# Performance work log

Hardware: AMD Instinct MI355X
Metric: run time of the kernel (lower is better)

## Reference

```python
import jax, jax.numpy as jnp
import numpy as np

N = 50000
E = 800000
IN_C = 128
HID = 16
HEADS = 8
OUT_C = 64
NEG_SLOPE = 0.2


def setup_inputs() -> dict:
    key = jax.random.key(0)
    ks = jax.random.split(key, 12)
    x = jax.random.normal(ks[0], (N, IN_C), dtype=jnp.float32)
    edge_index = jax.random.randint(ks[1], (2, E), 0, N, dtype=jnp.int32)
    s = 0.1
    W1 = jax.random.normal(ks[2], (IN_C, HEADS * HID), dtype=jnp.float32) * s
    a1_src = jax.random.normal(ks[3], (HEADS, HID), dtype=jnp.float32) * s
    a1_dst = jax.random.normal(ks[4], (HEADS, HID), dtype=jnp.float32) * s
    b1 = jnp.zeros((HEADS * HID,), dtype=jnp.float32)
    W2 = jax.random.normal(ks[5], (HEADS * HID, OUT_C), dtype=jnp.float32) * s
    a2_src = jax.random.normal(ks[6], (1, OUT_C), dtype=jnp.float32) * s
    a2_dst = jax.random.normal(ks[7], (1, OUT_C), dtype=jnp.float32) * s
    b2 = jnp.zeros((OUT_C,), dtype=jnp.float32)
    return {"x": x, "edge_index": edge_index, "W1": W1, "a1_src": a1_src,
            "a1_dst": a1_dst, "b1": b1, "W2": W2, "a2_src": a2_src,
            "a2_dst": a2_dst, "b2": b2}


def gat_conv(x, src, dst, W, a_src, a_dst, b, heads, ch):
    # linear projection -> [N, H, C]
    h = (x @ W).reshape(N, heads, ch)
    # per-node attention logits [N, H]
    al_s = jnp.einsum('nhc,hc->nh', h, a_src)
    al_d = jnp.einsum('nhc,hc->nh', h, a_dst)
    # per-edge logits [E, H]
    e = jax.nn.leaky_relu(al_s[src] + al_d[dst], NEG_SLOPE)
    # segment softmax over incoming edges of each dst node
    emax = jax.ops.segment_max(e, dst, num_segments=N)
    ee = jnp.exp(e - emax[dst])
    denom = jax.ops.segment_sum(ee, dst, num_segments=N)
    alpha = ee / (denom[dst] + 1e-16)
    # weighted scatter-aggregate of source messages
    msg = h[src] * alpha[:, :, None]  # [E, H, C]
    out = jax.ops.segment_sum(msg, dst, num_segments=N)
    return out.reshape(N, heads * ch) + b


def reference(x, edge_index, W1, a1_src, a1_dst, b1, W2, a2_src, a2_dst, b2):
    # add self loops (PyG GATConv default add_self_loops=True)
    loops = jnp.arange(N, dtype=edge_index.dtype)
    src = jnp.concatenate([edge_index[0], loops])
    dst = jnp.concatenate([edge_index[1], loops])
    h = gat_conv(x, src, dst, W1, a1_src, a1_dst, b1, HEADS, HID)
    h = jax.nn.relu(h)
    # dropout p=0.6 is identity in eval mode
    out = gat_conv(h, src, dst, W2, a2_src, a2_dst, b2, 1, OUT_C)
    return out
```

## Files before the change

### kernel.cpp

```cpp
#include <hip/hip_runtime.h>
#include <hip/hip_fp16.h>
#include <math.h>

#define N_NODES 50000
#define E_EDGES 800000
#define IN_C    128
#define HID     16
#define HEADS   8
#define OUT_C   64
#define NEG_SLOPE 0.2f
#define CELLW   64

#define WCOLS   144
#define WSTRIDE 136
#define WBYTES  (WCOLS * WSTRIDE * 2)

typedef _Float16 half8 __attribute__((ext_vector_type(8)));
typedef _Float16 half4 __attribute__((ext_vector_type(4)));
typedef float floatx4 __attribute__((ext_vector_type(4)));

__device__ __forceinline__ float lrelu_exp(float v) {
    v = v > 0.f ? v : NEG_SLOPE * v;
    return __expf(v);
}

__device__ __forceinline__ void gload_lds16(const void* g, void* l) {
    __builtin_amdgcn_global_load_lds(
        (const __attribute__((address_space(1))) void*)g,
        (__attribute__((address_space(3))) void*)l, 16, 0, 0);
}

__global__ __launch_bounds__(256) void prep(
    const float* __restrict__ W1, const float* __restrict__ a1_src,
    const float* __restrict__ a1_dst, const float* __restrict__ W2,
    _Float16* __restrict__ W1t, _Float16* __restrict__ W2t,
    int* __restrict__ cursor) {
    const int t = threadIdx.x;
    const int n = blockIdx.x * 256 + t;
    if (n < N_NODES) cursor[n] = 0;
    if (blockIdx.x == 0) {
        const int col = t & 127;
        const int kq = (t >> 7) * 4;
        for (int it = 0; it < 16; ++it) {
            const int k0 = it * 8 + kq;
            half4 hv;
            hv[0] = (_Float16)W1[(size_t)(k0 + 0) * IN_C + col];
            hv[1] = (_Float16)W1[(size_t)(k0 + 1) * IN_C + col];
            hv[2] = (_Float16)W1[(size_t)(k0 + 2) * IN_C + col];
            hv[3] = (_Float16)W1[(size_t)(k0 + 3) * IN_C + col];
            *(half4*)&W1t[col * WSTRIDE + k0] = hv;
        }
    } else if (blockIdx.x == 1) {
        const int j = t & 15;
        const int k0 = (t >> 4) * 8;
        const float* av = (j < 8) ? (a1_src + j * 16) : (a1_dst + (j - 8) * 16);
        const int hc = (j & 7) * 16;
        for (int k = k0; k < k0 + 8; ++k) {
            float s = 0.f;
#pragma unroll
            for (int c = 0; c < 16; ++c) s += W1[(size_t)k * IN_C + hc + c] * av[c];
            W1t[(128 + j) * WSTRIDE + k] = (_Float16)s;
        }
    } else if (blockIdx.x == 2) {
        const int col = t & 63;
        const int kg = t >> 6;
        for (int k0 = kg * 32; k0 < kg * 32 + 32; k0 += 4) {
            half4 hv;
            hv[0] = (_Float16)W2[(size_t)(k0 + 0) * OUT_C + col];
            hv[1] = (_Float16)W2[(size_t)(k0 + 1) * OUT_C + col];
            hv[2] = (_Float16)W2[(size_t)(k0 + 2) * OUT_C + col];
            hv[3] = (_Float16)W2[(size_t)(k0 + 3) * OUT_C + col];
            *(half4*)&W2t[col * 136 + k0] = hv;
        }
    }
}

__global__ __launch_bounds__(256) void fused_gemm_fill(
    const float* __restrict__ X, const _Float16* __restrict__ W1t,
    __half* __restrict__ H,
    float* __restrict__ als, float* __restrict__ ald,
    const int* __restrict__ src, const int* __restrict__ dst,
    int* __restrict__ cursor, int* __restrict__ ell) {
    __shared__ _Float16 wT[WCOLS * WSTRIDE];
    const int bid = blockIdx.x;
    const int t = threadIdx.x;

    if (bid & 1) {
        const int tid = (bid >> 1) * 256 + t;
        if (tid < E_EDGES / 4) {
            const int4 s4 = ((const int4*)src)[tid];
            const int4 d4 = ((const int4*)dst)[tid];
            const int p0 = atomicAdd(&cursor[d4.x], 1);
            const int p1 = atomicAdd(&cursor[d4.y], 1);
            const int p2 = atomicAdd(&cursor[d4.z], 1);
            const int p3 = atomicAdd(&cursor[d4.w], 1);
            if (p0 < CELLW) ell[(size_t)d4.x * CELLW + p0] = s4.x;
            if (p1 < CELLW) ell[(size_t)d4.y * CELLW + p1] = s4.y;
            if (p2 < CELLW) ell[(size_t)d4.z * CELLW + p2] = s4.z;
            if (p3 < CELLW) ell[(size_t)d4.w * CELLW + p3] = s4.w;
        }
        return;
    }

    {
        const char* g = (const char*)W1t;
        char* l = (char*)wT;
        const int o = t * 16;
#pragma unroll
        for (int it = 0; it < 9; ++it) {
            const int off = it * 4096 + o;
            gload_lds16(g + off, l + off);
        }
        if (t < 144) {
            const int off = 36864 + o;
            gload_lds16(g + off, l + off);
        }
    }

    const int wave = t >> 6, lane = t & 63;
    const int m = lane & 15, quad = lane >> 4;
    const int r0w = (bid >> 1) * 64 + wave * 16;
    int rl = r0w + m;
    if (rl >= N_NODES) rl = N_NODES - 1;
    const float* Xr = X + (size_t)rl * IN_C;

    float4 xv[8];
#pragma unroll
    for (int kc = 0; kc < 4; ++kc) {
        const int k8 = kc * 32 + quad * 8;
        xv[kc * 2]     = *(const float4*)(Xr + k8);
        xv[kc * 2 + 1] = *(const float4*)(Xr + k8 + 4);
    }

    __syncthreads();

    floatx4 acc[9];
#pragma unroll
    for (int i = 0; i < 9; ++i) acc[i] = (floatx4){0.f, 0.f, 0.f, 0.f};

#pragma unroll
    for (int kc = 0; kc < 4; ++kc) {
        const int k8 = kc * 32 + quad * 8;
        const float4 xa = xv[kc * 2];
        const float4 xb = xv[kc * 2 + 1];
        half8 a;
        a[0] = (_Float16)xa.x; a[1] = (_Float16)xa.y;
        a[2] = (_Float16)xa.z; a[3] = (_Float16)xa.w;
        a[4] = (_Float16)xb.x; a[5] = (_Float16)xb.y;
        a[6] = (_Float16)xb.z; a[7] = (_Float16)xb.w;
#pragma unroll
        for (int ct = 0; ct < 9; ++ct) {
            const half8 b = *(const half8*)&wT[(ct * 16 + m) * WSTRIDE + k8];
            acc[ct] = __builtin_amdgcn_mfma_f32_16x16x32_f16(a, b, acc[ct], 0, 0, 0);
        }
    }

    _Float16* Hh = (_Float16*)H;
#pragma unroll
    for (int ct = 0; ct < 8; ++ct) {
#pragma unroll
        for (int r = 0; r < 4; ++r) {
            const int row = r0w + quad * 4 + r;
            if (row < N_NODES)
                Hh[(size_t)row * IN_C + ct * 16 + m] = (_Float16)acc[ct][r];
        }
    }
#pragma unroll
    for (int r = 0; r < 4; ++r) {
        const int row = r0w + quad * 4 + r;
        if (row < N_NODES) {
            if (m < 8) als[(size_t)row * HEADS + m] = acc[8][r];
            else       ald[(size_t)row * HEADS + (m - 8)] = acc[8][r];
        }
    }
}

__global__ __launch_bounds__(256) void agg1_gemm2(
    const int* __restrict__ cnt, const int* __restrict__ ell,
    const float* __restrict__ als, const float* __restrict__ ald,
    const __half* __restrict__ H, const float* __restrict__ b,
    const _Float16* __restrict__ W2t, const float* __restrict__ a2_src,
    const float* __restrict__ a2_dst, __half* __restrict__ H2,
    float* __restrict__ als2, float* __restrict__ ald2) {
    __shared__ _Float16 xrowh[16 * 136];
    __shared__ float l2buf[4][16][2];
    const int t = threadIdx.x;

    const int nl = t >> 4;
    const int h  = (t >> 1) & 7;
    const int e2 = t & 1;
    const int nc = blockIdx.x * 16 + nl;
    int deg = cnt[nc];
    deg = deg < CELLW ? deg : CELLW;
    const int* ep = ell + (size_t)nc * CELLW;
    const float ad = ald[nc * HEADS + h];
    float accv[16];
    float ssum;
    if (e2 == 0) {
        const float w = lrelu_exp(als[nc * HEADS + h] + ad);
        const half8* q = (const half8*)(H + ((size_t)nc * HEADS + h) * HID);
        const half8 u0 = q[0], u1 = q[1];
        ssum = w;
#pragma unroll
        for (int j = 0; j < 8; ++j) {
            accv[j] = w * (float)u0[j];
            accv[j + 8] = w * (float)u1[j];
        }
    } else {
        ssum = 0.f;
#pragma unroll
        for (int j = 0; j < 16; ++j) accv[j] = 0.f;
    }
    for (int p = 4 * e2; p < deg; p += 8) {
        const int4 s4 = *(const int4*)(ep + p);
        const int s0 = s4.x;
        const int i1 = (p + 1 < deg) ? s4.y : nc;
        const int i2 = (p + 2 < deg) ? s4.z : nc;
        const int i3 = (p + 3 < deg) ? s4.w : nc;
        const float f1 = (p + 1 < deg) ? 1.f : 0.f;
        const float f2 = (p + 2 < deg) ? 1.f : 0.f;
        const float f3 = (p + 3 < deg) ? 1.f : 0.f;
        const float v0 = als[s0 * HEADS + h];
        const float v1 = als[i1 * HEADS + h];
        const float v2 = als[i2 * HEADS + h];
        const float v3 = als[i3 * HEADS + h];
        const half8* q0 = (const half8*)(H + ((size_t)s0 * HEADS + h) * HID);
        const half8* q1 = (const half8*)(H + ((size_t)i1 * HEADS + h) * HID);
        const half8* q2 = (const half8*)(H + ((size_t)i2 * HEADS + h) * HID);
        const half8* q3 = (const half8*)(H + ((size_t)i3 * HEADS + h) * HID);
        const half8 a0 = q0[0], b0 = q0[1];
        const half8 a1 = q1[0], b1 = q1[1];
        const half8 a2 = q2[0], b2 = q2[1];
        const half8 a3 = q3[0], b3 = q3[1];
        const float w0 = lrelu_exp(v0 + ad);
        const float w1 = lrelu_exp(v1 + ad) * f1;
        const float w2 = lrelu_exp(v2 + ad) * f2;
        const float w3 = lrelu_exp(v3 + ad) * f3;
        ssum += (w0 + w1) + (w2 + w3);
#pragma unroll
        for (int j = 0; j < 8; ++j) {
            accv[j]     += w0 * (float)a0[j] + w1 * (float)a1[j] +
                           w2 * (float)a2[j] + w3 * (float)a3[j];
            accv[j + 8] += w0 * (float)b0[j] + w1 * (float)b1[j] +
                           w2 * (float)b2[j] + w3 * (float)b3[j];
        }
    }
    ssum += __shfl_xor(ssum, 1);
#pragma unroll
    for (int j = 0; j < 16; ++j) accv[j] += __shfl_xor(accv[j], 1);

    if (e2 == 0) {
        const float inv = 1.f / (ssum + 1e-16f);
        half8 r0, r1;
#pragma unroll
        for (int j = 0; j < 8; ++j) {
            float ra = accv[j] * inv + b[h * 16 + j];
            float rb = accv[j + 8] * inv + b[h * 16 + 8 + j];
            r0[j] = (_Float16)(ra > 0.f ? ra : 0.f);
            r1[j] = (_Float16)(rb > 0.f ? rb : 0.f);
        }
        _Float16* xr = &xrowh[nl * 136 + h * 16];
        *(half8*)(xr) = r0;
        *(half8*)(xr + 8) = r1;
    }

    __syncthreads();

    {
        const int wv = t >> 6, ln = t & 63;
        const int bm = ln & 15, quad = ln >> 4;
        floatx4 acc = (floatx4){0.f, 0.f, 0.f, 0.f};
        const _Float16* arow = &xrowh[bm * 136];
        const _Float16* brow = &W2t[(wv * 16 + bm) * 136];
#pragma unroll
        for (int kc = 0; kc < 4; ++kc) {
            const int k8 = kc * 32 + quad * 8;
            const half8 a  = *(const half8*)(arow + k8);
            const half8 bv = *(const half8*)(brow + k8);
            acc = __builtin_amdgcn_mfma_f32_16x16x32_f16(a, bv, acc, 0, 0, 0);
        }
        const float a2s = a2_src[wv * 16 + bm], a2d = a2_dst[wv * 16 + bm];
        _Float16* H2h = (_Float16*)H2;
        float psr[4], pdr[4];
#pragma unroll
        for (int r = 0; r < 4; ++r) {
            const float c = acc[r];
            float ps = c * a2s, pd = c * a2d;
            ps += __shfl_xor(ps, 1); pd += __shfl_xor(pd, 1);
            ps += __shfl_xor(ps, 2); pd += __shfl_xor(pd, 2);
            ps += __shfl_xor(ps, 4); pd += __shfl_xor(pd, 4);
            ps += __shfl_xor(ps, 8); pd += __shfl_xor(pd, 8);
            psr[r] = ps; pdr[r] = pd;
            const int row = blockIdx.x * 16 + quad * 4 + r;
            H2h[(size_t)row * OUT_C + wv * 16 + bm] = (_Float16)c;
        }
        if (bm == 0) {
#pragma unroll
            for (int r = 0; r < 4; ++r) {
                l2buf[wv][quad * 4 + r][0] = psr[r];
                l2buf[wv][quad * 4 + r][1] = pdr[r];
            }
        }
    }
    __syncthreads();
    if (t < 16) {
        const int n2 = blockIdx.x * 16 + t;
        als2[n2] = (l2buf[0][t][0] + l2buf[1][t][0]) + (l2buf[2][t][0] + l2buf[3][t][0]);
        ald2[n2] = (l2buf[0][t][1] + l2buf[1][t][1]) + (l2buf[2][t][1] + l2buf[3][t][1]);
    }
}

__global__ __launch_bounds__(256) void agg2(
    const int* __restrict__ cnt, const int* __restrict__ ell,
    const float* __restrict__ als, const float* __restrict__ ald,
    const __half* __restrict__ H, const float* __restrict__ b,
    float* __restrict__ out) {
    const int t = threadIdx.x;
    const int nl = t >> 4;
    const int jc = (t >> 1) & 7;
    const int e2 = t & 1;
    const int n = blockIdx.x * 16 + nl;
    const int j0 = jc * 8;
    int deg = cnt[n];
    deg = deg < CELLW ? deg : CELLW;
    const int* ep = ell + (size_t)n * CELLW;
    const float ad = ald[n];
    float accv[8];
    float ssum;
    if (e2 == 0) {
        const float w = lrelu_exp(als[n] + ad);
        const half8 u = *(const half8*)(H + (size_t)n * OUT_C + j0);
        ssum = w;
#pragma unroll
        for (int k = 0; k < 8; ++k) accv[k] = w * (float)u[k];
    } else {
        ssum = 0.f;
#pragma unroll
        for (int k = 0; k < 8; ++k) accv[k] = 0.f;
    }
    for (int p = 4 * e2; p < deg; p += 8) {
        const int4 s4 = *(const int4*)(ep + p);
        const int s0 = s4.x;
        const int i1 = (p + 1 < deg) ? s4.y : n;
        const int i2 = (p + 2 < deg) ? s4.z : n;
        const int i3 = (p + 3 < deg) ? s4.w : n;
        const float f1 = (p + 1 < deg) ? 1.f : 0.f;
        const float f2 = (p + 2 < deg) ? 1.f : 0.f;
        const float f3 = (p + 3 < deg) ? 1.f : 0.f;
        const float v0 = als[s0];
        const float v1 = als[i1];
        const float v2 = als[i2];
        const float v3 = als[i3];
        const half8 u0 = *(const half8*)(H + (size_t)s0 * OUT_C + j0);
        const half8 u1 = *(const half8*)(H + (size_t)i1 * OUT_C + j0);
        const half8 u2 = *(const half8*)(H + (size_t)i2 * OUT_C + j0);
        const half8 u3 = *(const half8*)(H + (size_t)i3 * OUT_C + j0);
        const float w0 = lrelu_exp(v0 + ad);
        const float w1 = lrelu_exp(v1 + ad) * f1;
        const float w2 = lrelu_exp(v2 + ad) * f2;
        const float w3 = lrelu_exp(v3 + ad) * f3;
        ssum += (w0 + w1) + (w2 + w3);
#pragma unroll
        for (int k = 0; k < 8; ++k)
            accv[k] += w0 * (float)u0[k] + w1 * (float)u1[k] +
                       w2 * (float)u2[k] + w3 * (float)u3[k];
    }
    ssum += __shfl_xor(ssum, 1);
#pragma unroll
    for (int k = 0; k < 8; ++k) accv[k] += __shfl_xor(accv[k], 1);

    if (e2 == 0) {
        const float inv = 1.f / (ssum + 1e-16f);
        floatx4 r0, r1;
        r0[0] = accv[0] * inv + b[j0 + 0]; r0[1] = accv[1] * inv + b[j0 + 1];
        r0[2] = accv[2] * inv + b[j0 + 2]; r0[3] = accv[3] * inv + b[j0 + 3];
        r1[0] = accv[4] * inv + b[j0 + 4]; r1[1] = accv[5] * inv + b[j0 + 5];
        r1[2] = accv[6] * inv + b[j0 + 6]; r1[3] = accv[7] * inv + b[j0 + 7];
        float* op = out + (size_t)n * OUT_C + j0;
        __builtin_nontemporal_store(r0, (floatx4*)op);
        __builtin_nontemporal_store(r1, (floatx4*)(op + 4));
    }
}

extern "C" void kernel_launch(void* const* d_in, const int* in_sizes, int n_in,
                              void* d_out, int out_size, void* d_ws, size_t ws_size,
                              hipStream_t stream) {
    const float* x      = (const float*)d_in[0];
    const int*   ei     = (const int*)d_in[1];
    const float* W1     = (const float*)d_in[2];
    const float* a1_src = (const float*)d_in[3];
    const float* a1_dst = (const float*)d_in[4];
    const float* b1     = (const float*)d_in[5];
    const float* W2     = (const float*)d_in[6];
    const float* a2_src = (const float*)d_in[7];
    const float* a2_dst = (const float*)d_in[8];
    const float* b2     = (const float*)d_in[9];
    const int* src = ei;
    const int* dst = ei + E_EDGES;
    float* outp = (float*)d_out;

    char* wsb = (char*)d_ws;
    __half* h1   = (__half*)wsb;
    __half* h2   = h1 + (size_t)N_NODES * IN_C;
    float*  als1 = (float*)(h2 + (size_t)N_NODES * OUT_C);
    float*  ald1 = als1 + N_NODES * HEADS;
    float*  als2 = ald1 + N_NODES * HEADS;
    float*  ald2 = als2 + N_NODES;
    int*    cursor = (int*)(ald2 + N_NODES);
    int*    ell    = cursor + N_NODES;
    _Float16* W2t  = (_Float16*)(ell + (size_t)N_NODES * CELLW);

    _Float16* W1t = (_Float16*)als2;

    prep<<<(N_NODES + 255) / 256, 256, 0, stream>>>(
        W1, a1_src, a1_dst, W2, W1t, W2t, cursor);

    {
        const int gemm_blocks = (N_NODES + 63) / 64;
        fused_gemm_fill<<<gemm_blocks * 2, 256, 0, stream>>>(
            x, W1t, h1, als1, ald1, src, dst, cursor, ell);
    }

    agg1_gemm2<<<N_NODES / 16, 256, 0, stream>>>(
        cursor, ell, als1, ald1, h1, b1, W2t, a2_src, a2_dst, h2, als2, ald2);

    agg2<<<N_NODES / 16, 256, 0, stream>>>(
        cursor, ell, als2, ald2, h2, b2, outp);
}
```

Before: 188.4 us.

## Pad ELL rows with a zero-weight phantom node and rebalance GEMM/fill blocks

Fills the whole ELL adjacency with a phantom node index and gives that node zero features and -1e30 attention logits. The aggregation loops can then drop per-edge bounds checks and masking multiplies, since padded slots contribute exp(-huge)=0. The fused GEMM/fill kernel now has each GEMM block handle 128 rows in two passes, with two edge-fill blocks per GEMM block. The price is a full 12.8 MB write of the ELL buffer in the prep kernel, plus padded workspace offsets.

```diff
diff --git a/kernel.cpp b/kernel.cpp
--- a/kernel.cpp
+++ b/kernel.cpp
@@ -10,10 +10,10 @@
 #define OUT_C   64
 #define NEG_SLOPE 0.2f
 #define CELLW   64
+#define PHANTOM N_NODES
 
 #define WCOLS   144
 #define WSTRIDE 136
-#define WBYTES  (WCOLS * WSTRIDE * 2)
 
 typedef _Float16 half8 __attribute__((ext_vector_type(8)));
 typedef _Float16 half4 __attribute__((ext_vector_type(4)));
@@ -34,10 +34,19 @@
     const float* __restrict__ W1, const float* __restrict__ a1_src,
     const float* __restrict__ a1_dst, const float* __restrict__ W2,
     _Float16* __restrict__ W1t, _Float16* __restrict__ W2t,
-    int* __restrict__ cursor) {
+    int* __restrict__ cursor, int* __restrict__ ell,
+    __half* __restrict__ H1, __half* __restrict__ H2,
+    float* __restrict__ als1, float* __restrict__ ald1,
+    float* __restrict__ als2) {
     const int t = threadIdx.x;
-    const int n = blockIdx.x * 256 + t;
-    if (n < N_NODES) cursor[n] = 0;
+    const int gid = blockIdx.x * 256 + t;
+    if (gid < N_NODES) cursor[gid] = 0;
+    {
+        const int4 pv = make_int4(PHANTOM, PHANTOM, PHANTOM, PHANTOM);
+        int4* e4 = (int4*)ell;
+        const int tot = N_NODES * CELLW / 4;
+        for (int i = gid; i < tot; i += gridDim.x * 256) e4[i] = pv;
+    }
     if (blockIdx.x == 0) {
         const int col = t & 127;
         const int kq = (t >> 7) * 4;
@@ -72,6 +81,13 @@
             hv[3] = (_Float16)W2[(size_t)(k0 + 3) * OUT_C + col];
             *(half4*)&W2t[col * 136 + k0] = hv;
         }
+    } else if (blockIdx.x == 3) {
+        const int4 z = make_int4(0, 0, 0, 0);
+        if (t < 16)      ((int4*)(H1 + (size_t)PHANTOM * IN_C))[t] = z;
+        else if (t < 24) ((int4*)(H2 + (size_t)PHANTOM * OUT_C))[t - 16] = z;
+        else if (t < 32) als1[(size_t)PHANTOM * HEADS + (t - 24)] = -1e30f;
+        else if (t < 40) ald1[(size_t)PHANTOM * HEADS + (t - 32)] = -1e30f;
+        else if (t == 40) als2[PHANTOM] = -1e30f;
     }
 }
 
@@ -84,9 +100,11 @@
     __shared__ _Float16 wT[WCOLS * WSTRIDE];
     const int bid = blockIdx.x;
     const int t = threadIdx.x;
-
-    if (bid & 1) {
-        const int tid = (bid >> 1) * 256 + t;
+    const int role = bid % 3;
+
+    if (role) {
+        const int fid = (bid / 3) * 2 + (role - 1);
+        const int tid = fid * 256 + t;
         if (tid < E_EDGES / 4) {
             const int4 s4 = ((const int4*)src)[tid];
             const int4 d4 = ((const int4*)dst)[tid];
@@ -117,60 +135,110 @@
         }
     }
 
+    const int g = bid / 3;
     const int wave = t >> 6, lane = t & 63;
     const int m = lane & 15, quad = lane >> 4;
-    const int r0w = (bid >> 1) * 64 + wave * 16;
-    int rl = r0w + m;
-    if (rl >= N_NODES) rl = N_NODES - 1;
-    const float* Xr = X + (size_t)rl * IN_C;
-
+    _Float16* Hh = (_Float16*)H;
+
+    const int r0a = g * 128 + wave * 16;
+    int rla = r0a + m;
+    if (rla >= N_NODES) rla = N_NODES - 1;
+    const float* Xra = X + (size_t)rla * IN_C;
     float4 xv[8];
 #pragma unroll
     for (int kc = 0; kc < 4; ++kc) {
         const int k8 = kc * 32 + quad * 8;
-        xv[kc * 2]     = *(const float4*)(Xr + k8);
-        xv[kc * 2 + 1] = *(const float4*)(Xr + k8 + 4);
+        xv[kc * 2]     = *(const float4*)(Xra + k8);
+        xv[kc * 2 + 1] = *(const float4*)(Xra + k8 + 4);
     }
 
     __syncthreads();
 
-    floatx4 acc[9];
-#pragma unroll
-    for (int i = 0; i < 9; ++i) acc[i] = (floatx4){0.f, 0.f, 0.f, 0.f};
-
-#pragma unroll
-    for (int kc = 0; kc < 4; ++kc) {
-        const int k8 = kc * 32 + quad * 8;
-        const float4 xa = xv[kc * 2];
-        const float4 xb = xv[kc * 2 + 1];
-        half8 a;
-        a[0] = (_Float16)xa.x; a[1] = (_Float16)xa.y;
-        a[2] = (_Float16)xa.z; a[3] = (_Float16)xa.w;
-        a[4] = (_Float16)xb.x; a[5] = (_Float16)xb.y;
-        a[6] = (_Float16)xb.z; a[7] = (_Float16)xb.w;
-#pragma unroll
-        for (int ct = 0; ct < 9; ++ct) {
-            const half8 b = *(const half8*)&wT[(ct * 16 + m) * WSTRIDE + k8];
-            acc[ct] = __builtin_amdgcn_mfma_f32_16x16x32_f16(a, b, acc[ct], 0, 0, 0);
-        }
-    }
-
-    _Float16* Hh = (_Float16*)H;
-#pragma unroll
-    for (int ct = 0; ct < 8; ++ct) {
+    {
+        floatx4 acc[9];
+#pragma unroll
+        for (int i = 0; i < 9; ++i) acc[i] = (floatx4){0.f, 0.f, 0.f, 0.f};
+#pragma unroll
+        for (int kc = 0; kc < 4; ++kc) {
+            const int k8 = kc * 32 + quad * 8;
+            const float4 xa = xv[kc * 2];
+            const float4 xb = xv[kc * 2 + 1];
+            half8 a;
+            a[0] = (_Float16)xa.x; a[1] = (_Float16)xa.y;
+            a[2] = (_Float16)xa.z; a[3] = (_Float16)xa.w;
+            a[4] = (_Float16)xb.x; a[5] = (_Float16)xb.y;
+            a[6] = (_Float16)xb.z; a[7] = (_Float16)xb.w;
+#pragma unroll
+            for (int ct = 0; ct < 9; ++ct) {
+                const half8 b = *(const half8*)&wT[(ct * 16 + m) * WSTRIDE + k8];
+                acc[ct] = __builtin_amdgcn_mfma_f32_16x16x32_f16(a, b, acc[ct], 0, 0, 0);
+            }
+        }
+#pragma unroll
+        for (int ct = 0; ct < 8; ++ct) {
+#pragma unroll
+            for (int r = 0; r < 4; ++r) {
+                const int row = r0a + quad * 4 + r;
+                if (row < N_NODES)
+                    Hh[(size_t)row * IN_C + ct * 16 + m] = (_Float16)acc[ct][r];
+            }
+        }
 #pragma unroll
         for (int r = 0; r < 4; ++r) {
-            const int row = r0w + quad * 4 + r;
-            if (row < N_NODES)
-                Hh[(size_t)row * IN_C + ct * 16 + m] = (_Float16)acc[ct][r];
-        }
-    }
-#pragma unroll
-    for (int r = 0; r < 4; ++r) {
-        const int row = r0w + quad * 4 + r;
-        if (row < N_NODES) {
-            if (m < 8) als[(size_t)row * HEADS + m] = acc[8][r];
-            else       ald[(size_t)row * HEADS + (m - 8)] = acc[8][r];
+            const int row = r0a + quad * 4 + r;
+            if (row < N_NODES) {
+                if (m < 8) als[(size_t)row * HEADS + m] = acc[8][r];
+                else       ald[(size_t)row * HEADS + (m - 8)] = acc[8][r];
+            }
+        }
+    }
+
+    {
+        const int r0b = r0a + 64;
+        int rlb = r0b + m;
+        if (rlb >= N_NODES) rlb = N_NODES - 1;
+        const float* Xrb = X + (size_t)rlb * IN_C;
+#pragma unroll
+        for (int kc = 0; kc < 4; ++kc) {
+            const int k8 = kc * 32 + quad * 8;
+            xv[kc * 2]     = *(const float4*)(Xrb + k8);
+            xv[kc * 2 + 1] = *(const float4*)(Xrb + k8 + 4);
+        }
+        floatx4 acc[9];
+#pragma unroll
+        for (int i = 0; i < 9; ++i) acc[i] = (floatx4){0.f, 0.f, 0.f, 0.f};
+#pragma unroll
+        for (int kc = 0; kc < 4; ++kc) {
+            const int k8 = kc * 32 + quad * 8;
+            const float4 xa = xv[kc * 2];
+            const float4 xb = xv[kc * 2 + 1];
+            half8 a;
+            a[0] = (_Float16)xa.x; a[1] = (_Float16)xa.y;
+            a[2] = (_Float16)xa.z; a[3] = (_Float16)xa.w;
+            a[4] = (_Float16)xb.x; a[5] = (_Float16)xb.y;
+            a[6] = (_Float16)xb.z; a[7] = (_Float16)xb.w;
+#pragma unroll
+            for (int ct = 0; ct < 9; ++ct) {
+                const half8 b = *(const half8*)&wT[(ct * 16 + m) * WSTRIDE + k8];
+                acc[ct] = __builtin_amdgcn_mfma_f32_16x16x32_f16(a, b, acc[ct], 0, 0, 0);
+            }
+        }
+#pragma unroll
+        for (int ct = 0; ct < 8; ++ct) {
+#pragma unroll
+            for (int r = 0; r < 4; ++r) {
+                const int row = r0b + quad * 4 + r;
+                if (row < N_NODES)
+                    Hh[(size_t)row * IN_C + ct * 16 + m] = (_Float16)acc[ct][r];
+            }
+        }
+#pragma unroll
+        for (int r = 0; r < 4; ++r) {
+            const int row = r0b + quad * 4 + r;
+            if (row < N_NODES) {
+                if (m < 8) als[(size_t)row * HEADS + m] = acc[8][r];
+                else       ald[(size_t)row * HEADS + (m - 8)] = acc[8][r];
+            }
         }
     }
 }
@@ -213,29 +281,22 @@
     }
     for (int p = 4 * e2; p < deg; p += 8) {
         const int4 s4 = *(const int4*)(ep + p);
-        const int s0 = s4.x;
-        const int i1 = (p + 1 < deg) ? s4.y : nc;
-        const int i2 = (p + 2 < deg) ? s4.z : nc;
-        const int i3 = (p + 3 < deg) ? s4.w : nc;
-        const float f1 = (p + 1 < deg) ? 1.f : 0.f;
-        const float f2 = (p + 2 < deg) ? 1.f : 0.f;
-        const float f3 = (p + 3 < deg) ? 1.f : 0.f;
-        const float v0 = als[s0 * HEADS + h];
-        const float v1 = als[i1 * HEADS + h];
-        const float v2 = als[i2 * HEADS + h];
-        const float v3 = als[i3 * HEADS + h];
-        const half8* q0 = (const half8*)(H + ((size_t)s0 * HEADS + h) * HID);
-        const half8* q1 = (const half8*)(H + ((size_t)i1 * HEADS + h) * HID);
-        const half8* q2 = (const half8*)(H + ((size_t)i2 * HEADS + h) * HID);
-        const half8* q3 = (const half8*)(H + ((size_t)i3 * HEADS + h) * HID);
+        const float v0 = als[s4.x * HEADS + h];
+        const float v1 = als[s4.y * HEADS + h];
+        const float v2 = als[s4.z * HEADS + h];
+        const float v3 = als[s4.w * HEADS + h];
+        const half8* q0 = (const half8*)(H + ((size_t)s4.x * HEADS + h) * HID);
+        const half8* q1 = (const half8*)(H + ((size_t)s4.y * HEADS + h) * HID);
+        const half8* q2 = (const half8*)(H + ((size_t)s4.z * HEADS + h) * HID);
+        const half8* q3 = (const half8*)(H + ((size_t)s4.w * HEADS + h) * HID);
         const half8 a0 = q0[0], b0 = q0[1];
         const half8 a1 = q1[0], b1 = q1[1];
         const half8 a2 = q2[0], b2 = q2[1];
         const half8 a3 = q3[0], b3 = q3[1];
         const float w0 = lrelu_exp(v0 + ad);
-        const float w1 = lrelu_exp(v1 + ad) * f1;
-        const float w2 = lrelu_exp(v2 + ad) * f2;
-        const float w3 = lrelu_exp(v3 + ad) * f3;
+        const float w1 = lrelu_exp(v1 + ad);
+        const float w2 = lrelu_exp(v2 + ad);
+        const float w3 = lrelu_exp(v3 + ad);
         ssum += (w0 + w1) + (w2 + w3);
 #pragma unroll
         for (int j = 0; j < 8; ++j) {
@@ -340,25 +401,18 @@
     }
     for (int p = 4 * e2; p < deg; p += 8) {
         const int4 s4 = *(const int4*)(ep + p);
-        const int s0 = s4.x;
-        const int i1 = (p + 1 < deg) ? s4.y : n;
-        const int i2 = (p + 2 < deg) ? s4.z : n;
-        const int i3 = (p + 3 < deg) ? s4.w : n;
-        const float f1 = (p + 1 < deg) ? 1.f : 0.f;
-        const float f2 = (p + 2 < deg) ? 1.f : 0.f;
-        const float f3 = (p + 3 < deg) ? 1.f : 0.f;
-        const float v0 = als[s0];
-        const float v1 = als[i1];
-        const float v2 = als[i2];
-        const float v3 = als[i3];
-        const half8 u0 = *(const half8*)(H + (size_t)s0 * OUT_C + j0);
-        const half8 u1 = *(const half8*)(H + (size_t)i1 * OUT_C + j0);
-        const half8 u2 = *(const half8*)(H + (size_t)i2 * OUT_C + j0);
-        const half8 u3 = *(const half8*)(H + (size_t)i3 * OUT_C + j0);
+        const float v0 = als[s4.x];
+        const float v1 = als[s4.y];
+        const float v2 = als[s4.z];
+        const float v3 = als[s4.w];
+        const half8 u0 = *(const half8*)(H + (size_t)s4.x * OUT_C + j0);
+        const half8 u1 = *(const half8*)(H + (size_t)s4.y * OUT_C + j0);
+        const half8 u2 = *(const half8*)(H + (size_t)s4.z * OUT_C + j0);
+        const half8 u3 = *(const half8*)(H + (size_t)s4.w * OUT_C + j0);
         const float w0 = lrelu_exp(v0 + ad);
-        const float w1 = lrelu_exp(v1 + ad) * f1;
-        const float w2 = lrelu_exp(v2 + ad) * f2;
-        const float w3 = lrelu_exp(v3 + ad) * f3;
+        const float w1 = lrelu_exp(v1 + ad);
+        const float w2 = lrelu_exp(v2 + ad);
+        const float w3 = lrelu_exp(v3 + ad);
         ssum += (w0 + w1) + (w2 + w3);
 #pragma unroll
         for (int k = 0; k < 8; ++k)
@@ -401,11 +455,11 @@
 
     char* wsb = (char*)d_ws;
     __half* h1   = (__half*)wsb;
-    __half* h2   = h1 + (size_t)N_NODES * IN_C;
-    float*  als1 = (float*)(h2 + (size_t)N_NODES * OUT_C);
-    float*  ald1 = als1 + N_NODES * HEADS;
-    float*  als2 = ald1 + N_NODES * HEADS;
-    float*  ald2 = als2 + N_NODES;
+    __half* h2   = h1 + (size_t)(N_NODES + 1) * IN_C;
+    float*  als1 = (float*)(h2 + (size_t)(N_NODES + 1) * OUT_C);
+    float*  ald1 = als1 + (size_t)(N_NODES + 1) * HEADS;
+    float*  als2 = ald1 + (size_t)(N_NODES + 1) * HEADS;
+    float*  ald2 = als2 + (N_NODES + 16);
     int*    cursor = (int*)(ald2 + N_NODES);
     int*    ell    = cursor + N_NODES;
     _Float16* W2t  = (_Float16*)(ell + (size_t)N_NODES * CELLW);
@@ -413,11 +467,11 @@
     _Float16* W1t = (_Float16*)als2;
 
     prep<<<(N_NODES + 255) / 256, 256, 0, stream>>>(
-        W1, a1_src, a1_dst, W2, W1t, W2t, cursor);
-
-    {
-        const int gemm_blocks = (N_NODES + 63) / 64;
-        fused_gemm_fill<<<gemm_blocks * 2, 256, 0, stream>>>(
+        W1, a1_src, a1_dst, W2, W1t, W2t, cursor, ell, h1, h2, als1, ald1, als2);
+
+    {
+        const int gemm_blocks = (N_NODES + 127) / 128;
+        fused_gemm_fill<<<gemm_blocks * 3, 256, 0, stream>>>(
             x, W1t, h1, als1, ald1, src, dst, cursor, ell);
     }
 
```

Result: slower. 199.0 us (+5.7%).

## Use head-major feature layout and split layer-two GEMM into separate kernel

Applied to the files above, without the earlier changes.

Stores layer-1 features and attention logits head-major, so each aggregation block handles a single head over 128 nodes and its gathers touch a compact per-head slab that may fit better in cache. The fused aggregate+GEMM2 kernel is split into a gather kernel that writes the aggregated activations to a workspace and a standalone MFMA GEMM2 kernel. That GEMM2 also computes the layer-2 attention logits through extra folded W2·a2 columns, replacing the shuffle reductions. agg2 is likewise chunked per column group. The cost is an extra kernel launch and an extra round trip of the aggregated activations through global memory.

```diff
diff --git a/kernel.cpp b/kernel.cpp
--- a/kernel.cpp
+++ b/kernel.cpp
@@ -13,7 +13,7 @@
 
 #define WCOLS   144
 #define WSTRIDE 136
-#define WBYTES  (WCOLS * WSTRIDE * 2)
+#define W2COLS  80
 
 typedef _Float16 half8 __attribute__((ext_vector_type(8)));
 typedef _Float16 half4 __attribute__((ext_vector_type(4)));
@@ -33,6 +33,7 @@
 __global__ __launch_bounds__(256) void prep(
     const float* __restrict__ W1, const float* __restrict__ a1_src,
     const float* __restrict__ a1_dst, const float* __restrict__ W2,
+    const float* __restrict__ a2_src, const float* __restrict__ a2_dst,
     _Float16* __restrict__ W1t, _Float16* __restrict__ W2t,
     int* __restrict__ cursor) {
     const int t = threadIdx.x;
@@ -72,13 +73,25 @@
             hv[3] = (_Float16)W2[(size_t)(k0 + 3) * OUT_C + col];
             *(half4*)&W2t[col * 136 + k0] = hv;
         }
+    } else if (blockIdx.x == 3) {
+        if (t < 256) {
+            const int k = t & 127;
+            const float* av = (t < 128) ? a2_src : a2_dst;
+            float s = 0.f;
+#pragma unroll
+            for (int j = 0; j < 64; ++j) s += W2[(size_t)k * OUT_C + j] * av[j];
+            W2t[(64 + (t >> 7)) * 136 + k] = (_Float16)s;
+        }
+        if (t < 136) {
+            for (int c = 66; c < W2COLS; ++c) W2t[c * 136 + t] = (_Float16)0.f;
+        }
     }
 }
 
 __global__ __launch_bounds__(256) void fused_gemm_fill(
     const float* __restrict__ X, const _Float16* __restrict__ W1t,
-    __half* __restrict__ H,
-    float* __restrict__ als, float* __restrict__ ald,
+    _Float16* __restrict__ H1hm,
+    float* __restrict__ als1hm, float* __restrict__ ald1hm,
     const int* __restrict__ src, const int* __restrict__ dst,
     int* __restrict__ cursor, int* __restrict__ ell) {
     __shared__ _Float16 wT[WCOLS * WSTRIDE];
@@ -155,50 +168,48 @@
         }
     }
 
-    _Float16* Hh = (_Float16*)H;
 #pragma unroll
     for (int ct = 0; ct < 8; ++ct) {
 #pragma unroll
         for (int r = 0; r < 4; ++r) {
             const int row = r0w + quad * 4 + r;
             if (row < N_NODES)
-                Hh[(size_t)row * IN_C + ct * 16 + m] = (_Float16)acc[ct][r];
+                H1hm[((size_t)ct * N_NODES + row) * 16 + m] = (_Float16)acc[ct][r];
         }
     }
 #pragma unroll
     for (int r = 0; r < 4; ++r) {
         const int row = r0w + quad * 4 + r;
         if (row < N_NODES) {
-            if (m < 8) als[(size_t)row * HEADS + m] = acc[8][r];
-            else       ald[(size_t)row * HEADS + (m - 8)] = acc[8][r];
-        }
-    }
-}
-
-__global__ __launch_bounds__(256) void agg1_gemm2(
+            if (m < 8) als1hm[(size_t)m * N_NODES + row] = acc[8][r];
+            else       ald1hm[(size_t)(m - 8) * N_NODES + row] = acc[8][r];
+        }
+    }
+}
+
+__global__ __launch_bounds__(256) void agg1_gather(
     const int* __restrict__ cnt, const int* __restrict__ ell,
-    const float* __restrict__ als, const float* __restrict__ ald,
-    const __half* __restrict__ H, const float* __restrict__ b,
-    const _Float16* __restrict__ W2t, const float* __restrict__ a2_src,
-    const float* __restrict__ a2_dst, __half* __restrict__ H2,
-    float* __restrict__ als2, float* __restrict__ ald2) {
-    __shared__ _Float16 xrowh[16 * 136];
-    __shared__ float l2buf[4][16][2];
+    const float* __restrict__ als1hm, const float* __restrict__ ald1hm,
+    const _Float16* __restrict__ H1hm, const float* __restrict__ b,
+    _Float16* __restrict__ xagg) {
     const int t = threadIdx.x;
-
-    const int nl = t >> 4;
-    const int h  = (t >> 1) & 7;
-    const int e2 = t & 1;
-    const int nc = blockIdx.x * 16 + nl;
+    const int h = blockIdx.x & 7;
+    const int chunk = blockIdx.x >> 3;
+    const int nl = t >> 1, e2 = t & 1;
+    int nc = chunk * 128 + nl;
+    const bool valid = nc < N_NODES;
+    if (!valid) nc = N_NODES - 1;
     int deg = cnt[nc];
     deg = deg < CELLW ? deg : CELLW;
     const int* ep = ell + (size_t)nc * CELLW;
-    const float ad = ald[nc * HEADS + h];
+    const float* balse = als1hm + (size_t)h * N_NODES;
+    const _Float16* bH = H1hm + (size_t)h * N_NODES * 16;
+    const float ad = ald1hm[(size_t)h * N_NODES + nc];
     float accv[16];
     float ssum;
     if (e2 == 0) {
-        const float w = lrelu_exp(als[nc * HEADS + h] + ad);
-        const half8* q = (const half8*)(H + ((size_t)nc * HEADS + h) * HID);
+        const float w = lrelu_exp(balse[nc] + ad);
+        const half8* q = (const half8*)(bH + (size_t)nc * 16);
         const half8 u0 = q[0], u1 = q[1];
         ssum = w;
 #pragma unroll
@@ -220,14 +231,14 @@
         const float f1 = (p + 1 < deg) ? 1.f : 0.f;
         const float f2 = (p + 2 < deg) ? 1.f : 0.f;
         const float f3 = (p + 3 < deg) ? 1.f : 0.f;
-        const float v0 = als[s0 * HEADS + h];
-        const float v1 = als[i1 * HEADS + h];
-        const float v2 = als[i2 * HEADS + h];
-        const float v3 = als[i3 * HEADS + h];
-        const half8* q0 = (const half8*)(H + ((size_t)s0 * HEADS + h) * HID);
-        const half8* q1 = (const half8*)(H + ((size_t)i1 * HEADS + h) * HID);
-        const half8* q2 = (const half8*)(H + ((size_t)i2 * HEADS + h) * HID);
-        const half8* q3 = (const half8*)(H + ((size_t)i3 * HEADS + h) * HID);
+        const float v0 = balse[s0];
+        const float v1 = balse[i1];
+        const float v2 = balse[i2];
+        const float v3 = balse[i3];
+        const half8* q0 = (const half8*)(bH + (size_t)s0 * 16);
+        const half8* q1 = (const half8*)(bH + (size_t)i1 * 16);
+        const half8* q2 = (const half8*)(bH + (size_t)i2 * 16);
+        const half8* q3 = (const half8*)(bH + (size_t)i3 * 16);
         const half8 a0 = q0[0], b0 = q0[1];
         const half8 a1 = q1[0], b1 = q1[1];
         const half8 a2 = q2[0], b2 = q2[1];
@@ -249,7 +260,7 @@
 #pragma unroll
     for (int j = 0; j < 16; ++j) accv[j] += __shfl_xor(accv[j], 1);
 
-    if (e2 == 0) {
+    if (e2 == 0 && valid) {
         const float inv = 1.f / (ssum + 1e-16f);
         half8 r0, r1;
 #pragma unroll
@@ -259,77 +270,87 @@
             r0[j] = (_Float16)(ra > 0.f ? ra : 0.f);
             r1[j] = (_Float16)(rb > 0.f ? rb : 0.f);
         }
-        _Float16* xr = &xrowh[nl * 136 + h * 16];
+        _Float16* xr = xagg + ((size_t)h * N_NODES + nc) * 16;
         *(half8*)(xr) = r0;
         *(half8*)(xr + 8) = r1;
     }
-
-    __syncthreads();
-
-    {
-        const int wv = t >> 6, ln = t & 63;
-        const int bm = ln & 15, quad = ln >> 4;
-        floatx4 acc = (floatx4){0.f, 0.f, 0.f, 0.f};
-        const _Float16* arow = &xrowh[bm * 136];
-        const _Float16* brow = &W2t[(wv * 16 + bm) * 136];
-#pragma unroll
-        for (int kc = 0; kc < 4; ++kc) {
-            const int k8 = kc * 32 + quad * 8;
-            const half8 a  = *(const half8*)(arow + k8);
-            const half8 bv = *(const half8*)(brow + k8);
-            acc = __builtin_amdgcn_mfma_f32_16x16x32_f16(a, bv, acc, 0, 0, 0);
-        }
-        const float a2s = a2_src[wv * 16 + bm], a2d = a2_dst[wv * 16 + bm];
-        _Float16* H2h = (_Float16*)H2;
-        float psr[4], pdr[4];
+}
+
+__global__ __launch_bounds__(256) void gemm2(
+    const _Float16* __restrict__ xagg, const _Float16* __restrict__ W2t,
+    _Float16* __restrict__ H2cs, float* __restrict__ als2, float* __restrict__ ald2) {
+    const int t = threadIdx.x;
+    const int wave = t >> 6, lane = t & 63;
+    const int m = lane & 15, quad = lane >> 4;
+    const int r0w = blockIdx.x * 64 + wave * 16;
+    int rl = r0w + m;
+    if (rl >= N_NODES) rl = N_NODES - 1;
+
+    half8 av[4];
+#pragma unroll
+    for (int kc = 0; kc < 4; ++kc) {
+        const int hidx = 2 * kc + (quad >> 1);
+        const int off = (quad & 1) * 8;
+        av[kc] = *(const half8*)(xagg + ((size_t)hidx * N_NODES + rl) * 16 + off);
+    }
+
+    floatx4 acc[5];
+#pragma unroll
+    for (int i = 0; i < 5; ++i) acc[i] = (floatx4){0.f, 0.f, 0.f, 0.f};
+#pragma unroll
+    for (int kc = 0; kc < 4; ++kc) {
+        const int k8 = kc * 32 + quad * 8;
+#pragma unroll
+        for (int ct = 0; ct < 5; ++ct) {
+            const half8 bv = *(const half8*)&W2t[(ct * 16 + m) * 136 + k8];
+            acc[ct] = __builtin_amdgcn_mfma_f32_16x16x32_f16(av[kc], bv, acc[ct], 0, 0, 0);
+        }
+    }
+
+#pragma unroll
+    for (int ct = 0; ct < 4; ++ct) {
+        const int cg = ct * 2 + (m >> 3);
+        const int ch = m & 7;
 #pragma unroll
         for (int r = 0; r < 4; ++r) {
-            const float c = acc[r];
-            float ps = c * a2s, pd = c * a2d;
-            ps += __shfl_xor(ps, 1); pd += __shfl_xor(pd, 1);
-            ps += __shfl_xor(ps, 2); pd += __shfl_xor(pd, 2);
-            ps += __shfl_xor(ps, 4); pd += __shfl_xor(pd, 4);
-            ps += __shfl_xor(ps, 8); pd += __shfl_xor(pd, 8);
-            psr[r] = ps; pdr[r] = pd;
-            const int row = blockIdx.x * 16 + quad * 4 + r;
-            H2h[(size_t)row * OUT_C + wv * 16 + bm] = (_Float16)c;
-        }
-        if (bm == 0) {
-#pragma unroll
-            for (int r = 0; r < 4; ++r) {
-                l2buf[wv][quad * 4 + r][0] = psr[r];
-                l2buf[wv][quad * 4 + r][1] = pdr[r];
-            }
-        }
-    }
-    __syncthreads();
-    if (t < 16) {
-        const int n2 = blockIdx.x * 16 + t;
-        als2[n2] = (l2buf[0][t][0] + l2buf[1][t][0]) + (l2buf[2][t][0] + l2buf[3][t][0]);
-        ald2[n2] = (l2buf[0][t][1] + l2buf[1][t][1]) + (l2buf[2][t][1] + l2buf[3][t][1]);
+            const int row = r0w + quad * 4 + r;
+            if (row < N_NODES)
+                H2cs[((size_t)cg * N_NODES + row) * 8 + ch] = (_Float16)acc[ct][r];
+        }
+    }
+#pragma unroll
+    for (int r = 0; r < 4; ++r) {
+        const int row = r0w + quad * 4 + r;
+        if (row < N_NODES) {
+            if (m == 0) als2[row] = acc[4][r];
+            else if (m == 1) ald2[row] = acc[4][r];
+        }
     }
 }
 
 __global__ __launch_bounds__(256) void agg2(
     const int* __restrict__ cnt, const int* __restrict__ ell,
     const float* __restrict__ als, const float* __restrict__ ald,
-    const __half* __restrict__ H, const float* __restrict__ b,
+    const _Float16* __restrict__ H2cs, const float* __restrict__ b,
     float* __restrict__ out) {
     const int t = threadIdx.x;
-    const int nl = t >> 4;
-    const int jc = (t >> 1) & 7;
-    const int e2 = t & 1;
-    const int n = blockIdx.x * 16 + nl;
-    const int j0 = jc * 8;
+    const int cg = blockIdx.x & 7;
+    const int chunk = blockIdx.x >> 3;
+    const int nl = t >> 1, e2 = t & 1;
+    int n = chunk * 128 + nl;
+    const bool valid = n < N_NODES;
+    if (!valid) n = N_NODES - 1;
+    const int j0 = cg * 8;
     int deg = cnt[n];
     deg = deg < CELLW ? deg : CELLW;
     const int* ep = ell + (size_t)n * CELLW;
+    const _Float16* bH = H2cs + (size_t)cg * N_NODES * 8;
     const float ad = ald[n];
     float accv[8];
     float ssum;
     if (e2 == 0) {
         const float w = lrelu_exp(als[n] + ad);
-        const half8 u = *(const half8*)(H + (size_t)n * OUT_C + j0);
+        const half8 u = *(const half8*)(bH + (size_t)n * 8);
         ssum = w;
 #pragma unroll
         for (int k = 0; k < 8; ++k) accv[k] = w * (float)u[k];
@@ -351,10 +372,10 @@
         const float v1 = als[i1];
         const float v2 = als[i2];
         const float v3 = als[i3];
-        const half8 u0 = *(const half8*)(H + (size_t)s0 * OUT_C + j0);
-        const half8 u1 = *(const half8*)(H + (size_t)i1 * OUT_C + j0);
-        const half8 u2 = *(const half8*)(H + (size_t)i2 * OUT_C + j0);
-        const half8 u3 = *(const half8*)(H + (size_t)i3 * OUT_C + j0);
+        const half8 u0 = *(const half8*)(bH + (size_t)s0 * 8);
+        const half8 u1 = *(const half8*)(bH + (size_t)i1 * 8);
+        const half8 u2 = *(const half8*)(bH + (size_t)i2 * 8);
+        const half8 u3 = *(const half8*)(bH + (size_t)i3 * 8);
         const float w0 = lrelu_exp(v0 + ad);
         const float w1 = lrelu_exp(v1 + ad) * f1;
         const float w2 = lrelu_exp(v2 + ad) * f2;
@@ -369,7 +390,7 @@
 #pragma unroll
     for (int k = 0; k < 8; ++k) accv[k] += __shfl_xor(accv[k], 1);
 
-    if (e2 == 0) {
+    if (e2 == 0 && valid) {
         const float inv = 1.f / (ssum + 1e-16f);
         floatx4 r0, r1;
         r0[0] = accv[0] * inv + b[j0 + 0]; r0[1] = accv[1] * inv + b[j0 + 1];
@@ -400,30 +421,33 @@
     float* outp = (float*)d_out;
 
     char* wsb = (char*)d_ws;
-    __half* h1   = (__half*)wsb;
-    __half* h2   = h1 + (size_t)N_NODES * IN_C;
-    float*  als1 = (float*)(h2 + (size_t)N_NODES * OUT_C);
-    float*  ald1 = als1 + N_NODES * HEADS;
-    float*  als2 = ald1 + N_NODES * HEADS;
-    float*  ald2 = als2 + N_NODES;
-    int*    cursor = (int*)(ald2 + N_NODES);
-    int*    ell    = cursor + N_NODES;
-    _Float16* W2t  = (_Float16*)(ell + (size_t)N_NODES * CELLW);
-
-    _Float16* W1t = (_Float16*)als2;
+    _Float16* h1hm  = (_Float16*)wsb;
+    _Float16* xagg  = h1hm + (size_t)HEADS * N_NODES * 16;
+    _Float16* h2cs  = xagg + (size_t)HEADS * N_NODES * 16;
+    float* als1hm   = (float*)(h2cs + (size_t)8 * N_NODES * 8);
+    float* ald1hm   = als1hm + (size_t)HEADS * N_NODES;
+    float* als2     = ald1hm + (size_t)HEADS * N_NODES;
+    float* ald2     = als2 + N_NODES;
+    int* cursor     = (int*)(ald2 + N_NODES);
+    int* ell        = cursor + N_NODES;
+    _Float16* W1t   = (_Float16*)(ell + (size_t)N_NODES * CELLW);
+    _Float16* W2t   = W1t + WCOLS * WSTRIDE;
 
     prep<<<(N_NODES + 255) / 256, 256, 0, stream>>>(
-        W1, a1_src, a1_dst, W2, W1t, W2t, cursor);
+        W1, a1_src, a1_dst, W2, a2_src, a2_dst, W1t, W2t, cursor);
 
     {
         const int gemm_blocks = (N_NODES + 63) / 64;
         fused_gemm_fill<<<gemm_blocks * 2, 256, 0, stream>>>(
-            x, W1t, h1, als1, ald1, src, dst, cursor, ell);
-    }
-
-    agg1_gemm2<<<N_NODES / 16, 256, 0, stream>>>(
-        cursor, ell, als1, ald1, h1, b1, W2t, a2_src, a2_dst, h2, als2, ald2);
-
-    agg2<<<N_NODES / 16, 256, 0, stream>>>(
-        cursor, ell, als2, ald2, h2, b2, outp);
-}
+            x, W1t, h1hm, als1hm, ald1hm, src, dst, cursor, ell);
+    }
+
+    agg1_gather<<<8 * ((N_NODES + 127) / 128), 256, 0, stream>>>(
+        cursor, ell, als1hm, ald1hm, h1hm, b1, xagg);
+
+    gemm2<<<(N_NODES + 63) / 64, 256, 0, stream>>>(
+        xagg, W2t, h2cs, als2, ald2);
+
+    agg2<<<8 * ((N_NODES + 127) / 128), 256, 0, stream>>>(
+        cursor, ell, als2, ald2, h2cs, b2, outp);
+}
```

After: 269.4 us. 43.0% more time.

## Split neighbor lists over four lanes and fold layer-2 attention vectors into W2

Applied to the files above, without the earlier changes.

Both aggregation kernels now give each node/head or node/column group four lanes instead of two, each taking a strided quarter of the edge list, with an extra shuffle-reduce step. agg1_gemm2 moves to 512-thread blocks and agg2 to 8 nodes per block, which adds parallelism on the latency-bound gathers. The layer-2 attention logits are precomputed as two extra W2 columns (W2·a2_src, W2·a2_dst) so a fifth MFMA wave produces als2/ald2 directly, removing the shuffle reduction, LDS buffer and second barrier. W1t is moved out of the als2 region so it no longer aliases the buffer it now shares a kernel with. The cost is more shuffles and lanes that sit idle when degrees are low, and the attention logits are now rounded to fp16 inside the weights.

```diff
diff --git a/kernel.cpp b/kernel.cpp
--- a/kernel.cpp
+++ b/kernel.cpp
@@ -13,7 +13,7 @@
 
 #define WCOLS   144
 #define WSTRIDE 136
-#define WBYTES  (WCOLS * WSTRIDE * 2)
+#define W2COLS  80
 
 typedef _Float16 half8 __attribute__((ext_vector_type(8)));
 typedef _Float16 half4 __attribute__((ext_vector_type(4)));
@@ -33,6 +33,7 @@
 __global__ __launch_bounds__(256) void prep(
     const float* __restrict__ W1, const float* __restrict__ a1_src,
     const float* __restrict__ a1_dst, const float* __restrict__ W2,
+    const float* __restrict__ a2_src, const float* __restrict__ a2_dst,
     _Float16* __restrict__ W1t, _Float16* __restrict__ W2t,
     int* __restrict__ cursor) {
     const int t = threadIdx.x;
@@ -72,6 +73,18 @@
             hv[3] = (_Float16)W2[(size_t)(k0 + 3) * OUT_C + col];
             *(half4*)&W2t[col * 136 + k0] = hv;
         }
+    } else if (blockIdx.x == 3) {
+        if (t < 256) {
+            const int k = t & 127;
+            const float* av = (t < 128) ? a2_src : a2_dst;
+            float s = 0.f;
+#pragma unroll
+            for (int j = 0; j < 64; ++j) s += W2[(size_t)k * OUT_C + j] * av[j];
+            W2t[(64 + (t >> 7)) * 136 + k] = (_Float16)s;
+        }
+        if (t < 136) {
+            for (int c = 66; c < W2COLS; ++c) W2t[c * 136 + t] = (_Float16)0.f;
+        }
     }
 }
 
@@ -175,20 +188,18 @@
     }
 }
 
-__global__ __launch_bounds__(256) void agg1_gemm2(
+__global__ __launch_bounds__(512) void agg1_gemm2(
     const int* __restrict__ cnt, const int* __restrict__ ell,
     const float* __restrict__ als, const float* __restrict__ ald,
     const __half* __restrict__ H, const float* __restrict__ b,
-    const _Float16* __restrict__ W2t, const float* __restrict__ a2_src,
-    const float* __restrict__ a2_dst, __half* __restrict__ H2,
+    const _Float16* __restrict__ W2t, __half* __restrict__ H2,
     float* __restrict__ als2, float* __restrict__ ald2) {
     __shared__ _Float16 xrowh[16 * 136];
-    __shared__ float l2buf[4][16][2];
     const int t = threadIdx.x;
 
-    const int nl = t >> 4;
-    const int h  = (t >> 1) & 7;
-    const int e2 = t & 1;
+    const int nl = t >> 5;
+    const int h  = (t >> 2) & 7;
+    const int e4 = t & 3;
     const int nc = blockIdx.x * 16 + nl;
     int deg = cnt[nc];
     deg = deg < CELLW ? deg : CELLW;
@@ -196,7 +207,7 @@
     const float ad = ald[nc * HEADS + h];
     float accv[16];
     float ssum;
-    if (e2 == 0) {
+    if (e4 == 0) {
         const float w = lrelu_exp(als[nc * HEADS + h] + ad);
         const half8* q = (const half8*)(H + ((size_t)nc * HEADS + h) * HID);
         const half8 u0 = q[0], u1 = q[1];
@@ -211,7 +222,7 @@
 #pragma unroll
         for (int j = 0; j < 16; ++j) accv[j] = 0.f;
     }
-    for (int p = 4 * e2; p < deg; p += 8) {
+    for (int p = 4 * e4; p < deg; p += 16) {
         const int4 s4 = *(const int4*)(ep + p);
         const int s0 = s4.x;
         const int i1 = (p + 1 < deg) ? s4.y : nc;
@@ -246,10 +257,14 @@
         }
     }
     ssum += __shfl_xor(ssum, 1);
-#pragma unroll
-    for (int j = 0; j < 16; ++j) accv[j] += __shfl_xor(accv[j], 1);
-
-    if (e2 == 0) {
+    ssum += __shfl_xor(ssum, 2);
+#pragma unroll
+    for (int j = 0; j < 16; ++j) {
+        accv[j] += __shfl_xor(accv[j], 1);
+        accv[j] += __shfl_xor(accv[j], 2);
+    }
+
+    if (e4 == 0) {
         const float inv = 1.f / (ssum + 1e-16f);
         half8 r0, r1;
 #pragma unroll
@@ -266,7 +281,7 @@
 
     __syncthreads();
 
-    {
+    if (t < 320) {
         const int wv = t >> 6, ln = t & 63;
         const int bm = ln & 15, quad = ln >> 4;
         floatx4 acc = (floatx4){0.f, 0.f, 0.f, 0.f};
@@ -279,34 +294,17 @@
             const half8 bv = *(const half8*)(brow + k8);
             acc = __builtin_amdgcn_mfma_f32_16x16x32_f16(a, bv, acc, 0, 0, 0);
         }
-        const float a2s = a2_src[wv * 16 + bm], a2d = a2_dst[wv * 16 + bm];
         _Float16* H2h = (_Float16*)H2;
-        float psr[4], pdr[4];
 #pragma unroll
         for (int r = 0; r < 4; ++r) {
-            const float c = acc[r];
-            float ps = c * a2s, pd = c * a2d;
-            ps += __shfl_xor(ps, 1); pd += __shfl_xor(pd, 1);
-            ps += __shfl_xor(ps, 2); pd += __shfl_xor(pd, 2);
-            ps += __shfl_xor(ps, 4); pd += __shfl_xor(pd, 4);
-            ps += __shfl_xor(ps, 8); pd += __shfl_xor(pd, 8);
-            psr[r] = ps; pdr[r] = pd;
             const int row = blockIdx.x * 16 + quad * 4 + r;
-            H2h[(size_t)row * OUT_C + wv * 16 + bm] = (_Float16)c;
-        }
-        if (bm == 0) {
-#pragma unroll
-            for (int r = 0; r < 4; ++r) {
-                l2buf[wv][quad * 4 + r][0] = psr[r];
-                l2buf[wv][quad * 4 + r][1] = pdr[r];
+            if (wv < 4) {
+                H2h[(size_t)row * OUT_C + wv * 16 + bm] = (_Float16)acc[r];
+            } else {
+                if (bm == 0)      als2[row] = acc[r];
+                else if (bm == 1) ald2[row] = acc[r];
             }
         }
-    }
-    __syncthreads();
-    if (t < 16) {
-        const int n2 = blockIdx.x * 16 + t;
-        als2[n2] = (l2buf[0][t][0] + l2buf[1][t][0]) + (l2buf[2][t][0] + l2buf[3][t][0]);
-        ald2[n2] = (l2buf[0][t][1] + l2buf[1][t][1]) + (l2buf[2][t][1] + l2buf[3][t][1]);
     }
 }
 
@@ -316,10 +314,10 @@
     const __half* __restrict__ H, const float* __restrict__ b,
     float* __restrict__ out) {
     const int t = threadIdx.x;
-    const int nl = t >> 4;
-    const int jc = (t >> 1) & 7;
-    const int e2 = t & 1;
-    const int n = blockIdx.x * 16 + nl;
+    const int nl = t >> 5;
+    const int jc = (t >> 2) & 7;
+    const int e4 = t & 3;
+    const int n = blockIdx.x * 8 + nl;
     const int j0 = jc * 8;
     int deg = cnt[n];
     deg = deg < CELLW ? deg : CELLW;
@@ -327,7 +325,7 @@
     const float ad = ald[n];
     float accv[8];
     float ssum;
-    if (e2 == 0) {
+    if (e4 == 0) {
         const float w = lrelu_exp(als[n] + ad);
         const half8 u = *(const half8*)(H + (size_t)n * OUT_C + j0);
         ssum = w;
@@ -338,7 +336,7 @@
 #pragma unroll
         for (int k = 0; k < 8; ++k) accv[k] = 0.f;
     }
-    for (int p = 4 * e2; p < deg; p += 8) {
+    for (int p = 4 * e4; p < deg; p += 16) {
         const int4 s4 = *(const int4*)(ep + p);
         const int s0 = s4.x;
         const int i1 = (p + 1 < deg) ? s4.y : n;
@@ -366,10 +364,14 @@
                        w2 * (float)u2[k] + w3 * (float)u3[k];
     }
     ssum += __shfl_xor(ssum, 1);
-#pragma unroll
-    for (int k = 0; k < 8; ++k) accv[k] += __shfl_xor(accv[k], 1);
-
-    if (e2 == 0) {
+    ssum += __shfl_xor(ssum, 2);
+#pragma unroll
+    for (int k = 0; k < 8; ++k) {
+        accv[k] += __shfl_xor(accv[k], 1);
+        accv[k] += __shfl_xor(accv[k], 2);
+    }
+
+    if (e4 == 0) {
         const float inv = 1.f / (ssum + 1e-16f);
         floatx4 r0, r1;
         r0[0] = accv[0] * inv + b[j0 + 0]; r0[1] = accv[1] * inv + b[j0 + 1];
@@ -403,17 +405,16 @@
     __half* h1   = (__half*)wsb;
     __half* h2   = h1 + (size_t)N_NODES * IN_C;
     float*  als1 = (float*)(h2 + (size_t)N_NODES * OUT_C);
-    float*  ald1 = als1 + N_NODES * HEADS;
-    float*  als2 = ald1 + N_NODES * HEADS;
+    float*  ald1 = als1 + (size_t)N_NODES * HEADS;
+    float*  als2 = ald1 + (size_t)N_NODES * HEADS;
     float*  ald2 = als2 + N_NODES;
     int*    cursor = (int*)(ald2 + N_NODES);
     int*    ell    = cursor + N_NODES;
-    _Float16* W2t  = (_Float16*)(ell + (size_t)N_NODES * CELLW);
-
-    _Float16* W1t = (_Float16*)als2;
+    _Float16* W1t  = (_Float16*)(ell + (size_t)N_NODES * CELLW);
+    _Float16* W2t  = W1t + WCOLS * WSTRIDE;
 
     prep<<<(N_NODES + 255) / 256, 256, 0, stream>>>(
-        W1, a1_src, a1_dst, W2, W1t, W2t, cursor);
+        W1, a1_src, a1_dst, W2, a2_src, a2_dst, W1t, W2t, cursor);
 
     {
         const int gemm_blocks = (N_NODES + 63) / 64;
@@ -421,9 +422,9 @@
             x, W1t, h1, als1, ald1, src, dst, cursor, ell);
     }
 
-    agg1_gemm2<<<N_NODES / 16, 256, 0, stream>>>(
-        cursor, ell, als1, ald1, h1, b1, W2t, a2_src, a2_dst, h2, als2, ald2);
-
-    agg2<<<N_NODES / 16, 256, 0, stream>>>(
+    agg1_gemm2<<<N_NODES / 16, 512, 0, stream>>>(
+        cursor, ell, als1, ald1, h1, b1, W2t, h2, als2, ald2);
+
+    agg2<<<N_NODES / 8, 256, 0, stream>>>(
         cursor, ell, als2, ald2, h2, b2, outp);
 }
```

After: 205.3 us. +9.0%, slower.
